# Kernel tuning notes

Hardware: AMD Instinct MI355X
Metric: run time of the kernel (lower is better)

Reference implementation:

```python
import jax, jax.numpy as jnp
import numpy as np

B, T, S, G, D, H, W, CHUNK = 2, 4096, 4096, 64, 1024, 16, 512, 256
HD = D // H


def setup_inputs() -> dict:
    key = jax.random.key(0)
    ks = jax.random.split(key, 16)
    std = 1.0 / np.sqrt(D)
    w = lambda k: jax.random.normal(k, (D, D), jnp.float32) * std
    b = lambda k: jax.random.normal(k, (D,), jnp.float32) * 0.01
    return {
        "query": jax.random.normal(ks[0], (B, T, D), jnp.float32),
        "encoder_out": jax.random.normal(ks[1], (B, S, D), jnp.float32),
        "global_tokens": jax.random.normal(ks[2], (B, G, D), jnp.float32),
        "qw": w(ks[3]), "qb": b(ks[4]),
        "kw": w(ks[5]), "kb": b(ks[6]),
        "vw": w(ks[7]), "vb": b(ks[8]),
        "gkw": w(ks[9]), "gkb": b(ks[10]),
        "gvw": w(ks[11]), "gvb": b(ks[12]),
        "ow": w(ks[13]), "ob": b(ks[14]),
        "compression_ratio": 1,
    }


def reference(query, encoder_out, global_tokens, qw, qb, kw, kb, vw, vb,
              gkw, gkb, gvw, gvb, ow, ob, compression_ratio):
    scale = jnp.float32(np.sqrt(HD))
    r = jnp.float32(compression_ratio)
    # expected raw position for each decoder step, clamped to valid src range
    expected = jnp.clip((jnp.arange(T, dtype=jnp.float32) / r).astype(jnp.int32), 0, S - 1)
    expected = jnp.broadcast_to(expected[None], (B, T))  # [B,T]

    lin = lambda x, wt, bs: x @ wt.T + bs  # torch nn.Linear: y = x W^T + b
    q = lin(query, qw, qb).reshape(B, T, H, HD).transpose(0, 2, 1, 3)            # [B,H,T,HD]
    gk = lin(global_tokens, gkw, gkb).reshape(B, G, H, HD).transpose(0, 2, 1, 3)  # [B,H,G,HD]
    gv = lin(global_tokens, gvw, gvb).reshape(B, G, H, HD).transpose(0, 2, 1, 3)
    ak = lin(encoder_out, kw, kb).reshape(B, S, H, HD).transpose(0, 2, 1, 3)      # [B,H,S,HD]
    av = lin(encoder_out, vw, vb).reshape(B, S, H, HD).transpose(0, 2, 1, 3)

    nC = T // CHUNK
    # per-(batch,chunk) window start, from the middle query's expected position
    centers = expected.reshape(B, nC, CHUNK)[:, :, CHUNK // 2]   # [B,nC]
    win_start = jnp.clip(centers - W // 2, 0, S - W)             # [B,nC]; window always full length W
    idx = win_start[:, :, None] + jnp.arange(W)[None, None, :]   # [B,nC,W]

    gather = lambda kv_b, idx_b: kv_b[:, idx_b, :]               # [H,S,HD],[nC,W] -> [H,nC,W,HD]
    wk = jax.vmap(gather)(ak, idx)                               # [B,H,nC,W,HD]
    wv = jax.vmap(gather)(av, idx)

    qc = q.reshape(B, H, nC, CHUNK, HD)
    sg = jnp.einsum('bhcqd,bhgd->bhcqg', qc, gk) / scale          # global scores  [B,H,nC,CHUNK,G]
    sl = jnp.einsum('bhcqd,bhcwd->bhcqw', qc, wk) / scale         # windowed scores [B,H,nC,CHUNK,W]
    attn = jax.nn.softmax(jnp.concatenate([sg, sl], axis=-1), axis=-1)
    out = (jnp.einsum('bhcqg,bhgd->bhcqd', attn[..., :G], gv)
           + jnp.einsum('bhcqw,bhcwd->bhcqd', attn[..., G:], wv))  # [B,H,nC,CHUNK,HD]
    out = out.reshape(B, H, T, HD).transpose(0, 2, 1, 3).reshape(B, T, D)
    return lin(out, ow, ob)
```

## Files before the change

### kernel.cpp

```cpp
#include <hip/hip_runtime.h>

typedef unsigned short u16;
typedef unsigned int u32;
typedef __attribute__((ext_vector_type(4))) float f32x4;
typedef __attribute__((ext_vector_type(16))) float f32x16;
typedef __attribute__((ext_vector_type(8))) short bf16x8;

constexpr int B_ = 2, T_ = 4096, S_ = 4096, G_ = 64, D_ = 1024, H_ = 16, W_ = 512, CHUNK_ = 256;
constexpr int NC_ = T_ / CHUNK_;
constexpr int NT_ = (G_ + W_) / 32;

__device__ __forceinline__ u16 f2bf(float x) {
  u32 u = __builtin_bit_cast(u32, x);
  return (u16)((u + 0x7FFFu + ((u >> 16) & 1u)) >> 16);
}

__global__ __launch_bounds__(256) void cvt_all_kernel(const float* __restrict__ q, const float* __restrict__ e,
                                                      const float* __restrict__ g, const float* __restrict__ w0,
                                                      const float* __restrict__ w1, const float* __restrict__ w2,
                                                      const float* __restrict__ w3, const float* __restrict__ w4,
                                                      const float* __restrict__ w5, u16* __restrict__ dst) {
  int blk = blockIdx.x;
  const float* src;
  int sblk;
  if (blk < 8192) { src = q; sblk = 0; }
  else if (blk < 16384) { src = e; sblk = 8192; }
  else if (blk < 16512) { src = g; sblk = 16384; }
  else if (blk < 17536) { src = w0; sblk = 16512; }
  else if (blk < 18560) { src = w1; sblk = 17536; }
  else if (blk < 19584) { src = w2; sblk = 18560; }
  else if (blk < 20608) { src = w3; sblk = 19584; }
  else if (blk < 21632) { src = w4; sblk = 20608; }
  else { src = w5; sblk = 21632; }
  int li = (blk - sblk) * 256 + threadIdx.x;
  size_t gi = (size_t)blk * 256 + threadIdx.x;
  float4 v = ((const float4*)src)[li];
  uint2 o;
  o.x = (u32)f2bf(v.x) | ((u32)f2bf(v.y) << 16);
  o.y = (u32)f2bf(v.z) | ((u32)f2bf(v.w) << 16);
  ((uint2*)dst)[gi] = o;
}

template <int MODE>
__global__ __launch_bounds__(256) void gemm_kernel(const u16* __restrict__ A, const u16* __restrict__ Bt,
                                                   const float* __restrict__ bias, const float* __restrict__ bias2,
                                                   size_t split, void* __restrict__ out) {
  __shared__ char lds[32768];
  char* As = lds;
  char* Bs = lds + 16384;
  const int tid = threadIdx.x;
  const int lane = tid & 63;
  const int wv = tid >> 6;
  const int wr = wv >> 1, wc = wv & 1;
  const int l15 = lane & 15, kg = lane >> 4;
  const int row0 = blockIdx.x * 128;
  const int col0 = blockIdx.y * 128;

  f32x4 acc[4][4];
#pragma unroll
  for (int i = 0; i < 4; i++)
#pragma unroll
    for (int j = 0; j < 4; j++)
#pragma unroll
      for (int r = 0; r < 4; r++) acc[i][j][r] = 0.f;

  const char* Abase = (const char*)A;
  const char* Bbase = (const char*)Bt;

  const int kb = 16 * ((lane & 3) ^ ((lane >> 3) & 3));
  auto stage = [&](int bufsel, int k0) {
#pragma unroll
    for (int c = 0; c < 2; c++) {
      int arow = wv * 32 + c * 16 + (lane >> 2);
      int dsto = bufsel * 8192 + wv * 2048 + c * 1024 + lane * 16;
      const char* ga = Abase + ((size_t)(row0 + arow) * 2048 + (size_t)k0 * 2 + kb);
      __builtin_amdgcn_global_load_lds((const __attribute__((address_space(1))) void*)ga,
                                       (__attribute__((address_space(3))) void*)(As + dsto), 16, 0, 0);
      const char* gb = Bbase + ((size_t)(col0 + arow) * 2048 + (size_t)k0 * 2 + kb);
      __builtin_amdgcn_global_load_lds((const __attribute__((address_space(1))) void*)gb,
                                       (__attribute__((address_space(3))) void*)(Bs + dsto), 16, 0, 0);
    }
  };

  stage(0, 0);
  __syncthreads();

  for (int it = 0; it < 32; ++it) {
    const int cur = it & 1;
    if (it + 1 < 32) stage(cur ^ 1, (it + 1) * 32);

    const char* Ab = As + cur * 8192;
    const char* Bb = Bs + cur * 8192;
    bf16x8 af[4], bfv[4];
#pragma unroll
    for (int mi = 0; mi < 4; mi++) {
      int row = wr * 64 + mi * 16 + l15;
      af[mi] = *(const bf16x8*)(Ab + ((row * 64 + kg * 16) ^ ((row & 6) << 3)));
    }
#pragma unroll
    for (int ni = 0; ni < 4; ni++) {
      int row = wc * 64 + ni * 16 + l15;
      bfv[ni] = *(const bf16x8*)(Bb + ((row * 64 + kg * 16) ^ ((row & 6) << 3)));
    }
    __builtin_amdgcn_s_setprio(1);
#pragma unroll
    for (int mi = 0; mi < 4; mi++)
#pragma unroll
      for (int ni = 0; ni < 4; ni++)
        acc[mi][ni] = __builtin_amdgcn_mfma_f32_16x16x32_bf16(bfv[ni], af[mi], acc[mi][ni], 0, 0, 0);
    __builtin_amdgcn_s_setprio(0);
    __syncthreads();
  }

  const float* bp = bias;
  size_t obase = 0;
  if (MODE == 3 && col0 >= 1024) {
    bp = bias2 - 1024;
    obase = split - 1024;
  }
  float4 bv4[4];
#pragma unroll
  for (int ni = 0; ni < 4; ni++) bv4[ni] = *(const float4*)&bp[col0 + wc * 64 + ni * 16 + kg * 4];
#pragma unroll
  for (int mi = 0; mi < 4; mi++) {
    size_t grow = (size_t)(row0 + wr * 64 + mi * 16 + l15);
#pragma unroll
    for (int ni = 0; ni < 4; ni++) {
      int gcol = col0 + wc * 64 + ni * 16 + kg * 4;
      float v0 = acc[mi][ni][0] + bv4[ni].x;
      float v1 = acc[mi][ni][1] + bv4[ni].y;
      float v2 = acc[mi][ni][2] + bv4[ni].z;
      float v3 = acc[mi][ni][3] + bv4[ni].w;
      if (MODE == 1) {
        v0 *= 0.18033688011112042f; v1 *= 0.18033688011112042f;
        v2 *= 0.18033688011112042f; v3 *= 0.18033688011112042f;
      }
      if (MODE == 2) {
        float4 fo = {v0, v1, v2, v3};
        *(float4*)&((float*)out)[grow * 1024 + gcol] = fo;
      } else {
        uint2 o;
        asm("v_cvt_pk_bf16_f32 %0, %1, %2" : "=v"(o.x) : "v"(v0), "v"(v1));
        asm("v_cvt_pk_bf16_f32 %0, %1, %2" : "=v"(o.y) : "v"(v2), "v"(v3));
        *(uint2*)&((u16*)out)[obase + grow * 1024 + gcol] = o;
      }
    }
  }
}

template <int MODE>
__global__ __launch_bounds__(512, 2) void gemm256_kernel(const u16* __restrict__ A, const u16* __restrict__ Bt,
                                                         const float* __restrict__ bias, const float* __restrict__ bias2,
                                                         size_t split, void* __restrict__ out) {
  __shared__ char lds[98304];
  const int tid = threadIdx.x;
  const int lane = tid & 63;
  const int wid = tid >> 6;
  const int wm = wid >> 2, wn = wid & 3;
  const int l15 = lane & 15, kg = lane >> 4;
  const int bid = blockIdx.x;
  const int swz = (bid & 7) * 32 + (bid >> 3);
  const int row0 = (swz & 31) * 256;
  const int col0 = (swz >> 5) * 256;

  f32x4 acc[8][4];
#pragma unroll
  for (int i = 0; i < 8; i++)
#pragma unroll
    for (int j = 0; j < 4; j++)
#pragma unroll
      for (int r = 0; r < 4; r++) acc[i][j][r] = 0.f;

  const char* Abase = (const char*)A;
  const char* Bbase = (const char*)Bt;
  const int kb = 16 * ((tid & 3) ^ ((tid >> 3) & 3));
  const int rl0 = tid >> 2;

  auto stageOp = [&](const char* base, int rowbase, int ldsbase, int kt) {
#pragma unroll
    for (int j = 0; j < 2; j++) {
      int dst = ldsbase + tid * 16 + j * 8192;
      const char* g = base + (size_t)(rowbase + rl0 + j * 128) * 2048 + kt * 64 + kb;
      __builtin_amdgcn_global_load_lds((const __attribute__((address_space(1))) void*)g,
                                       (__attribute__((address_space(3))) void*)(lds + dst), 16, 0, 0);
    }
  };

  stageOp(Abase, row0, 0, 0);
  stageOp(Bbase, col0, 49152, 0);
  stageOp(Abase, row0, 16384, 1);
  stageOp(Bbase, col0, 49152 + 16384, 1);
  asm volatile("s_waitcnt vmcnt(4)" ::: "memory");
  __builtin_amdgcn_s_barrier();

  int cur = 0, nx = 2;
  for (int t = 0; t < 32; ++t) {
    const char* Ab = lds + cur * 16384;
    const char* Bb = lds + 49152 + cur * 16384;
    bf16x8 bfv[4], af[4];
#pragma unroll
    for (int ni = 0; ni < 4; ni++) {
      int r = wn * 64 + ni * 16 + l15;
      bfv[ni] = *(const bf16x8*)(Bb + ((r * 64 + kg * 16) ^ (((r >> 1) & 3) << 4)));
    }
#pragma unroll
    for (int mi = 0; mi < 4; mi++) {
      int r = wm * 128 + mi * 16 + l15;
      af[mi] = *(const bf16x8*)(Ab + ((r * 64 + kg * 16) ^ (((r >> 1) & 3) << 4)));
    }
    if (t + 2 < 32) stageOp(Abase, row0, nx * 16384, t + 2);
    __builtin_amdgcn_s_barrier();
    __builtin_amdgcn_s_setprio(1);
#pragma unroll
    for (int mi = 0; mi < 4; mi++)
#pragma unroll
      for (int ni = 0; ni < 4; ni++)
        acc[mi][ni] = __builtin_amdgcn_mfma_f32_16x16x32_bf16(bfv[ni], af[mi], acc[mi][ni], 0, 0, 0);
    __builtin_amdgcn_s_setprio(0);
    __builtin_amdgcn_s_barrier();
#pragma unroll
    for (int mi = 0; mi < 4; mi++) {
      int r = wm * 128 + (mi + 4) * 16 + l15;
      af[mi] = *(const bf16x8*)(Ab + ((r * 64 + kg * 16) ^ (((r >> 1) & 3) << 4)));
    }
    if (t + 2 < 32) stageOp(Bbase, col0, 49152 + nx * 16384, t + 2);
    __builtin_amdgcn_s_barrier();
    __builtin_amdgcn_s_setprio(1);
#pragma unroll
    for (int mi = 0; mi < 4; mi++)
#pragma unroll
      for (int ni = 0; ni < 4; ni++)
        acc[mi + 4][ni] = __builtin_amdgcn_mfma_f32_16x16x32_bf16(bfv[ni], af[mi], acc[mi + 4][ni], 0, 0, 0);
    __builtin_amdgcn_s_setprio(0);
    if (t < 30) {
      asm volatile("s_waitcnt vmcnt(4)" ::: "memory");
    } else if (t == 30) {
      asm volatile("s_waitcnt vmcnt(0)" ::: "memory");
    }
    __builtin_amdgcn_s_barrier();
    cur = cur == 2 ? 0 : cur + 1;
    nx = nx == 2 ? 0 : nx + 1;
  }

  const float* bp = bias;
  size_t obase = 0;
  if (MODE == 3 && col0 >= 1024) {
    bp = bias2 - 1024;
    obase = split - 1024;
  }
  float4 bv4[4];
#pragma unroll
  for (int ni = 0; ni < 4; ni++) bv4[ni] = *(const float4*)&bp[col0 + wn * 64 + ni * 16 + kg * 4];
#pragma unroll
  for (int mi = 0; mi < 8; mi++) {
    size_t grow = (size_t)(row0 + wm * 128 + mi * 16 + l15);
#pragma unroll
    for (int ni = 0; ni < 4; ni++) {
      int gcol = col0 + wn * 64 + ni * 16 + kg * 4;
      float v0 = acc[mi][ni][0] + bv4[ni].x;
      float v1 = acc[mi][ni][1] + bv4[ni].y;
      float v2 = acc[mi][ni][2] + bv4[ni].z;
      float v3 = acc[mi][ni][3] + bv4[ni].w;
      if (MODE == 1) {
        v0 *= 0.18033688011112042f; v1 *= 0.18033688011112042f;
        v2 *= 0.18033688011112042f; v3 *= 0.18033688011112042f;
      }
      if (MODE == 2) {
        float4 fo = {v0, v1, v2, v3};
        *(float4*)&((float*)out)[grow * 1024 + gcol] = fo;
      } else {
        uint2 o;
        asm("v_cvt_pk_bf16_f32 %0, %1, %2" : "=v"(o.x) : "v"(v0), "v"(v1));
        asm("v_cvt_pk_bf16_f32 %0, %1, %2" : "=v"(o.y) : "v"(v2), "v"(v3));
        *(uint2*)&((u16*)out)[obase + grow * 1024 + gcol] = o;
      }
    }
  }
}

__global__ __launch_bounds__(512, 4) void attn_kernel(const u16* __restrict__ q_bf, const u16* __restrict__ k_bf,
                                                      const u16* __restrict__ v_bf, const u16* __restrict__ gk_bf,
                                                      const u16* __restrict__ gv_bf, u16* __restrict__ ao,
                                                      const int* __restrict__ rptr) {
  __shared__ u16 smem[16384];
  const int c = blockIdx.x, h = blockIdx.y, b = blockIdx.z;
  const int tid = threadIdx.x;
  const int lane = tid & 63, wv = tid >> 6;
  const int l31 = lane & 31, half = lane >> 5;
  const int t0 = c * CHUNK_;

  int rr = rptr[0];
  int centert = c * CHUNK_ + CHUNK_ / 2;
  int expected = (int)((float)centert / (float)rr);
  expected = min(max(expected, 0), S_ - 1);
  int ws0 = min(max(expected - W_ / 2, 0), S_ - W_);

  bf16x8 qf[4];
  {
    const u16* qrow = q_bf + ((size_t)(b * T_ + t0 + wv * 32 + l31)) * D_ + h * 64 + half * 8;
#pragma unroll
    for (int s = 0; s < 4; s++) qf[s] = *(const bf16x8*)(qrow + s * 16);
  }

  const int skey = (tid & 255) >> 3, shq = tid & 7;
  const bool isK = tid < 256;

  auto load_tile = [&](int j) -> uint4 {
    const u16* base;
    size_t row;
    if (j < 2) {
      base = isK ? gk_bf : gv_bf;
      row = (size_t)(b * G_ + j * 32 + skey);
    } else {
      base = isK ? k_bf : v_bf;
      row = (size_t)(b * S_ + ws0 + (j - 2) * 32 + skey);
    }
    return *(const uint4*)(base + row * D_ + h * 64 + shq * 8);
  };

  f32x16 oacc[2];
#pragma unroll
  for (int i = 0; i < 2; i++)
#pragma unroll
    for (int r = 0; r < 16; r++) oacc[i][r] = 0.f;
  float mrun = -1e30f, lsum = 0.f;

  uint4 stg = load_tile(0);

  for (int j = 0; j < NT_; j++) {
    const int bsel = j & 1;
    if (isK) {
      *(uint4*)((char*)smem + bsel * 4096 + ((skey * 128 + shq * 16) ^ ((skey & 7) << 4))) = stg;
    } else {
      const u16* pv = (const u16*)&stg;
      char* bp = (char*)smem + 8192 + bsel * 5248 + shq * 656 + skey * 2;
#pragma unroll
      for (int e = 0; e < 8; e++) *(u16*)(bp + e * 80) = pv[e];
    }
    if (j + 1 < NT_) stg = load_tile(j + 1);
    __syncthreads();

    const int kbase = bsel * 4096;
    const int vtb = 8192 + bsel * 5248;

    f32x16 sacc;
#pragma unroll
    for (int r = 0; r < 16; r++) sacc[r] = 0.f;
    __builtin_amdgcn_s_setprio(1);
#pragma unroll
    for (int s = 0; s < 4; s++) {
      int kbx = kbase + ((l31 * 128 + half * 16 + s * 32) ^ ((l31 & 7) << 4));
      bf16x8 kf = *(const bf16x8*)((char*)smem + kbx);
      sacc = __builtin_amdgcn_mfma_f32_32x32x16_bf16(kf, qf[s], sacc, 0, 0, 0);
    }
    __builtin_amdgcn_s_setprio(0);

    float t0m = fmaxf(fmaxf(sacc[0], sacc[1]), sacc[2]);
    float t1m = fmaxf(fmaxf(sacc[3], sacc[4]), sacc[5]);
    float t2m = fmaxf(fmaxf(sacc[6], sacc[7]), sacc[8]);
    float t3m = fmaxf(fmaxf(sacc[9], sacc[10]), sacc[11]);
    float t4m = fmaxf(fmaxf(sacc[12], sacc[13]), sacc[14]);
    float tmax = fmaxf(fmaxf(fmaxf(t0m, t1m), fmaxf(t2m, t3m)), fmaxf(t4m, sacc[15]));
    tmax = fmaxf(tmax, __shfl_xor(tmax, 32));
    if (__any(tmax > mrun + 8.f)) {
      float mnew = fmaxf(mrun, tmax);
      float fac = __builtin_amdgcn_exp2f(mrun - mnew);
      mrun = mnew;
      lsum *= fac;
#pragma unroll
      for (int i = 0; i < 2; i++)
#pragma unroll
        for (int r = 0; r < 16; r++) oacc[i][r] *= fac;
    }
    float p[16];
#pragma unroll
    for (int r = 0; r < 16; r++) p[r] = __builtin_amdgcn_exp2f(sacc[r] - mrun);
    float s0s = (p[0] + p[1]) + (p[2] + p[3]);
    float s1s = (p[4] + p[5]) + (p[6] + p[7]);
    float s2s = (p[8] + p[9]) + (p[10] + p[11]);
    float s3s = (p[12] + p[13]) + (p[14] + p[15]);
    float tsum = (s0s + s1s) + (s2s + s3s);
    tsum += __shfl_xor(tsum, 32);
    lsum += tsum;

    u32 xs[8], px[8];
#pragma unroll
    for (int i = 0; i < 8; i++)
      asm("v_cvt_pk_bf16_f32 %0, %1, %2" : "=v"(xs[i]) : "v"(p[2 * i]), "v"(p[2 * i + 1]));
#pragma unroll
    for (int i = 0; i < 8; i++) px[i] = (u32)__shfl_xor((int)xs[i], 32);
    u32 Bk[2][4];
    Bk[0][0] = half ? px[2] : xs[0];
    Bk[0][1] = half ? px[3] : xs[1];
    Bk[0][2] = half ? xs[2] : px[0];
    Bk[0][3] = half ? xs[3] : px[1];
    Bk[1][0] = half ? px[6] : xs[4];
    Bk[1][1] = half ? px[7] : xs[5];
    Bk[1][2] = half ? xs[6] : px[4];
    Bk[1][3] = half ? xs[7] : px[5];

    int vro = vtb + l31 * 80 + ((l31 >> 3) << 4) + half * 16;
    __builtin_amdgcn_s_setprio(1);
#pragma unroll
    for (int hdf = 0; hdf < 2; hdf++) {
#pragma unroll
      for (int ks = 0; ks < 2; ks++) {
        bf16x8 vf = *(const bf16x8*)((const char*)smem + vro + hdf * 2624 + ks * 32);
        uint4 u4;
        u4.x = Bk[ks][0]; u4.y = Bk[ks][1]; u4.z = Bk[ks][2]; u4.w = Bk[ks][3];
        bf16x8 pb = __builtin_bit_cast(bf16x8, u4);
        oacc[hdf] = __builtin_amdgcn_mfma_f32_32x32x16_bf16(vf, pb, oacc[hdf], 0, 0, 0);
      }
    }
    __builtin_amdgcn_s_setprio(0);
  }

  __syncthreads();
  float inv = 1.f / lsum;
#pragma unroll
  for (int hdf = 0; hdf < 2; hdf++) {
#pragma unroll
    for (int a = 0; a < 4; a++) {
      float f0 = oacc[hdf][4 * a] * inv, f1 = oacc[hdf][4 * a + 1] * inv;
      float f2 = oacc[hdf][4 * a + 2] * inv, f3 = oacc[hdf][4 * a + 3] * inv;
      uint2 o;
      asm("v_cvt_pk_bf16_f32 %0, %1, %2" : "=v"(o.x) : "v"(f0), "v"(f1));
      asm("v_cvt_pk_bf16_f32 %0, %1, %2" : "=v"(o.y) : "v"(f2), "v"(f3));
      int off = wv * 4096 + l31 * 128 + ((16 * a + 8 * half + 64 * hdf) ^ ((l31 & 7) << 4));
      *(uint2*)((char*)smem + off) = o;
    }
  }
  __syncthreads();
#pragma unroll
  for (int it = 0; it < 4; it++) {
    int byteo = (tid + it * 512) * 16;
    int row = byteo >> 7;
    int colb = byteo & 127;
    uint4 vv = *(const uint4*)((const char*)smem + row * 128 + (colb ^ ((row & 7) << 4)));
    *(uint4*)(ao + ((size_t)(b * T_ + t0 + row)) * D_ + h * 64 + (colb >> 1)) = vv;
  }
}

extern "C" void kernel_launch(void* const* d_in, const int* in_sizes, int n_in,
                              void* d_out, int out_size, void* d_ws, size_t ws_size,
                              hipStream_t stream) {
  (void)in_sizes; (void)n_in; (void)out_size; (void)ws_size;
  const float* query = (const float*)d_in[0];
  const float* enc = (const float*)d_in[1];
  const float* glob = (const float*)d_in[2];
  const float* qw = (const float*)d_in[3];
  const float* qb = (const float*)d_in[4];
  const float* kw = (const float*)d_in[5];
  const float* kb = (const float*)d_in[6];
  const float* vw = (const float*)d_in[7];
  const float* vb = (const float*)d_in[8];
  const float* gkw = (const float*)d_in[9];
  const float* gkb = (const float*)d_in[10];
  const float* gvw = (const float*)d_in[11];
  const float* gvb = (const float*)d_in[12];
  const float* ow = (const float*)d_in[13];
  const float* ob = (const float*)d_in[14];
  const int* rp = (const int*)d_in[15];

  const size_t NQ = (size_t)B_ * T_ * D_;
  const size_t NG = (size_t)B_ * G_ * D_;
  const size_t NW = (size_t)D_ * D_;

  u16* ws = (u16*)d_ws;
  u16* qx = ws;
  u16* ex = qx + NQ;
  u16* gx = ex + NQ;
  u16* wgt = gx + NG;
  u16* q_bf = wgt + 6 * NW;
  u16* k_bf = q_bf + NQ;
  u16* v_bf = k_bf + NQ;
  u16* gk_bf = v_bf + NQ;
  u16* gv_bf = gk_bf + NG;
  u16* ao = gv_bf + NG;

  cvt_all_kernel<<<22656, 256, 0, stream>>>(query, enc, glob, qw, kw, vw, gkw, gvw, ow, ws);

  gemm_kernel<1><<<dim3(64, 8), 256, 0, stream>>>(qx, wgt + 0 * NW, qb, qb, 0, q_bf);
  gemm256_kernel<3><<<256, 512, 0, stream>>>(ex, wgt + 1 * NW, kb, vb, NQ, k_bf);
  gemm_kernel<3><<<dim3(1, 16), 256, 0, stream>>>(gx, wgt + 3 * NW, gkb, gvb, NG, gk_bf);

  attn_kernel<<<dim3(NC_, H_, B_), 512, 0, stream>>>(q_bf, k_bf, v_bf, gk_bf, gv_bf, ao, rp);

  gemm_kernel<2><<<dim3(64, 8), 256, 0, stream>>>(ao, wgt + 5 * NW, ob, ob, 0, d_out);
}
```

Before: 164.2 us.

## Merge Q, K/V and global-token projections into one grouped GEMM launch

The separate Q projection GEMM, the 256x256-tile K/V GEMM and the small global-token GEMM are replaced by a single proj_kernel launch of 784 blocks. Each block picks its operand set, bias and output from its block index and computes a 256x128 tile with a triple-buffered direct-to-LDS pipeline. The aim is to remove launch gaps and fill the tail of one GEMM with work from the others. In exchange, K/V now uses smaller 128-column tiles with less B reuse. The global-token tile stages 256 rows of A while only 128 exist, so it reads past the gx buffer into adjacent workspace and discards those rows.

```diff
diff --git a/kernel.cpp b/kernel.cpp
--- a/kernel.cpp
+++ b/kernel.cpp
@@ -41,6 +41,163 @@
   ((uint2*)dst)[gi] = o;
 }
 
+__global__ __launch_bounds__(256, 2) void proj_kernel(const u16* __restrict__ ex, const u16* __restrict__ qx,
+                                                      const u16* __restrict__ gx, const u16* __restrict__ wgt,
+                                                      const float* __restrict__ qb, const float* __restrict__ kbias,
+                                                      const float* __restrict__ vbias, const float* __restrict__ gkb,
+                                                      const float* __restrict__ gvb, u16* __restrict__ q_bf,
+                                                      u16* __restrict__ k_bf, u16* __restrict__ gk_bf) {
+  __shared__ char lds[73728];
+  constexpr size_t NW = (size_t)D_ * D_;
+  constexpr size_t NQs = (size_t)B_ * T_ * D_;
+  constexpr size_t NGs = (size_t)B_ * G_ * D_;
+  const int tid = threadIdx.x;
+  const int lane = tid & 63;
+  const int wid = tid >> 6;
+  const int wm = wid >> 1, wn = wid & 1;
+  const int l15 = lane & 15, kg = lane >> 4;
+
+  const int bid = blockIdx.x;
+  const u16 *A, *Bt;
+  const float *b1, *b2;
+  u16* out;
+  int row0, col0, mloc;
+  bool scale = false, dual = false;
+  size_t dsplit = 0;
+  if (bid < 512) {
+    row0 = (bid & 31) * 256; col0 = (bid >> 5) * 128; mloc = 256;
+    A = ex; Bt = wgt + NW; b1 = kbias; b2 = vbias; out = k_bf; dsplit = NQs; dual = true;
+  } else if (bid < 768) {
+    int i = bid - 512;
+    row0 = (i & 31) * 256; col0 = (i >> 5) * 128; mloc = 256;
+    A = qx; Bt = wgt; b1 = qb; b2 = qb; out = q_bf; scale = true;
+  } else {
+    int i = bid - 768;
+    row0 = 0; col0 = i * 128; mloc = 128;
+    A = gx; Bt = wgt + 3 * NW; b1 = gkb; b2 = gvb; out = gk_bf; dsplit = NGs; dual = true;
+  }
+  const float* bp = b1;
+  u16* op = out;
+  if (dual && col0 >= 1024) { bp = b2 - 1024; op = out + (dsplit - 1024); }
+
+  f32x4 acc[8][4];
+#pragma unroll
+  for (int i = 0; i < 8; i++)
+#pragma unroll
+    for (int j = 0; j < 4; j++)
+#pragma unroll
+      for (int r = 0; r < 4; r++) acc[i][j][r] = 0.f;
+
+  const char* Abase = (const char*)A;
+  const char* Bbase = (const char*)Bt;
+  const int swb = 16 * ((tid & 3) ^ ((tid >> 3) & 3));
+
+  auto stageA = [&](int slot, int kt) {
+#pragma unroll
+    for (int p = 0; p < 4; p++) {
+      int dst = slot * 16384 + p * 4096 + tid * 16;
+      const char* g = Abase + (size_t)(row0 + p * 64 + (tid >> 2)) * 2048 + kt * 64 + swb;
+      __builtin_amdgcn_global_load_lds((const __attribute__((address_space(1))) void*)g,
+                                       (__attribute__((address_space(3))) void*)(lds + dst), 16, 0, 0);
+    }
+  };
+  auto stageB = [&](int slot, int kt) {
+#pragma unroll
+    for (int p = 0; p < 2; p++) {
+      int dst = 49152 + slot * 8192 + p * 4096 + tid * 16;
+      const char* g = Bbase + (size_t)(col0 + p * 64 + (tid >> 2)) * 2048 + kt * 64 + swb;
+      __builtin_amdgcn_global_load_lds((const __attribute__((address_space(1))) void*)g,
+                                       (__attribute__((address_space(3))) void*)(lds + dst), 16, 0, 0);
+    }
+  };
+
+  stageA(0, 0); stageB(0, 0);
+  stageA(1, 1); stageB(1, 1);
+  asm volatile("s_waitcnt vmcnt(6)" ::: "memory");
+  __builtin_amdgcn_s_barrier();
+
+  int cur = 0, nx = 2;
+  for (int t = 0; t < 32; ++t) {
+    const char* Ab = lds + cur * 16384;
+    const char* Bb = lds + 49152 + cur * 8192;
+    bf16x8 bfv[2], af[4];
+#pragma unroll
+    for (int ni = 0; ni < 2; ni++) {
+      int r = wn * 64 + ni * 16 + l15;
+      (void)r;
+    }
+    bf16x8 bq[4];
+#pragma unroll
+    for (int ni = 0; ni < 4; ni++) {
+      int r = wn * 64 + ni * 16 + l15;
+      bq[ni] = *(const bf16x8*)(Bb + ((r * 64 + kg * 16) ^ (((r >> 1) & 3) << 4)));
+    }
+#pragma unroll
+    for (int mi = 0; mi < 4; mi++) {
+      int r = wm * 128 + mi * 16 + l15;
+      af[mi] = *(const bf16x8*)(Ab + ((r * 64 + kg * 16) ^ (((r >> 1) & 3) << 4)));
+    }
+    if (t + 2 < 32) stageA(nx, t + 2);
+    __builtin_amdgcn_s_barrier();
+    __builtin_amdgcn_s_setprio(1);
+#pragma unroll
+    for (int mi = 0; mi < 4; mi++)
+#pragma unroll
+      for (int ni = 0; ni < 4; ni++)
+        acc[mi][ni] = __builtin_amdgcn_mfma_f32_16x16x32_bf16(bq[ni], af[mi], acc[mi][ni], 0, 0, 0);
+    __builtin_amdgcn_s_setprio(0);
+    __builtin_amdgcn_s_barrier();
+#pragma unroll
+    for (int mi = 0; mi < 4; mi++) {
+      int r = wm * 128 + (mi + 4) * 16 + l15;
+      af[mi] = *(const bf16x8*)(Ab + ((r * 64 + kg * 16) ^ (((r >> 1) & 3) << 4)));
+    }
+    if (t + 2 < 32) stageB(nx, t + 2);
+    __builtin_amdgcn_s_barrier();
+    __builtin_amdgcn_s_setprio(1);
+#pragma unroll
+    for (int mi = 0; mi < 4; mi++)
+#pragma unroll
+      for (int ni = 0; ni < 4; ni++)
+        acc[mi + 4][ni] = __builtin_amdgcn_mfma_f32_16x16x32_bf16(bq[ni], af[mi], acc[mi + 4][ni], 0, 0, 0);
+    __builtin_amdgcn_s_setprio(0);
+    if (t < 30) {
+      asm volatile("s_waitcnt vmcnt(6)" ::: "memory");
+    } else if (t == 30) {
+      asm volatile("s_waitcnt vmcnt(0)" ::: "memory");
+    }
+    __builtin_amdgcn_s_barrier();
+    cur = cur == 2 ? 0 : cur + 1;
+    nx = nx == 2 ? 0 : nx + 1;
+  }
+
+  float4 bv4[4];
+#pragma unroll
+  for (int ni = 0; ni < 4; ni++) bv4[ni] = *(const float4*)&bp[col0 + wn * 64 + ni * 16 + kg * 4];
+#pragma unroll
+  for (int mi = 0; mi < 8; mi++) {
+    int rloc = wm * 128 + mi * 16 + l15;
+    if (rloc >= mloc) continue;
+    size_t grow = (size_t)(row0 + rloc);
+#pragma unroll
+    for (int ni = 0; ni < 4; ni++) {
+      int gcol = col0 + wn * 64 + ni * 16 + kg * 4;
+      float v0 = acc[mi][ni][0] + bv4[ni].x;
+      float v1 = acc[mi][ni][1] + bv4[ni].y;
+      float v2 = acc[mi][ni][2] + bv4[ni].z;
+      float v3 = acc[mi][ni][3] + bv4[ni].w;
+      if (scale) {
+        v0 *= 0.18033688011112042f; v1 *= 0.18033688011112042f;
+        v2 *= 0.18033688011112042f; v3 *= 0.18033688011112042f;
+      }
+      uint2 o;
+      asm("v_cvt_pk_bf16_f32 %0, %1, %2" : "=v"(o.x) : "v"(v0), "v"(v1));
+      asm("v_cvt_pk_bf16_f32 %0, %1, %2" : "=v"(o.y) : "v"(v2), "v"(v3));
+      *(uint2*)&op[grow * 1024 + gcol] = o;
+    }
+  }
+}
+
 template <int MODE>
 __global__ __launch_bounds__(256) void gemm_kernel(const u16* __restrict__ A, const u16* __restrict__ Bt,
                                                    const float* __restrict__ bias, const float* __restrict__ bias2,
@@ -113,11 +270,7 @@
   }
 
   const float* bp = bias;
-  size_t obase = 0;
-  if (MODE == 3 && col0 >= 1024) {
-    bp = bias2 - 1024;
-    obase = split - 1024;
-  }
+  (void)bias2; (void)split;
   float4 bv4[4];
 #pragma unroll
   for (int ni = 0; ni < 4; ni++) bv4[ni] = *(const float4*)&bp[col0 + wc * 64 + ni * 16 + kg * 4];
@@ -131,10 +284,6 @@
       float v1 = acc[mi][ni][1] + bv4[ni].y;
       float v2 = acc[mi][ni][2] + bv4[ni].z;
       float v3 = acc[mi][ni][3] + bv4[ni].w;
-      if (MODE == 1) {
-        v0 *= 0.18033688011112042f; v1 *= 0.18033688011112042f;
-        v2 *= 0.18033688011112042f; v3 *= 0.18033688011112042f;
-      }
       if (MODE == 2) {
         float4 fo = {v0, v1, v2, v3};
         *(float4*)&((float*)out)[grow * 1024 + gcol] = fo;
@@ -142,137 +291,7 @@
         uint2 o;
         asm("v_cvt_pk_bf16_f32 %0, %1, %2" : "=v"(o.x) : "v"(v0), "v"(v1));
         asm("v_cvt_pk_bf16_f32 %0, %1, %2" : "=v"(o.y) : "v"(v2), "v"(v3));
-        *(uint2*)&((u16*)out)[obase + grow * 1024 + gcol] = o;
-      }
-    }
-  }
-}
-
-template <int MODE>
-__global__ __launch_bounds__(512, 2) void gemm256_kernel(const u16* __restrict__ A, const u16* __restrict__ Bt,
-                                                         const float* __restrict__ bias, const float* __restrict__ bias2,
-                                                         size_t split, void* __restrict__ out) {
-  __shared__ char lds[98304];
-  const int tid = threadIdx.x;
-  const int lane = tid & 63;
-  const int wid = tid >> 6;
-  const int wm = wid >> 2, wn = wid & 3;
-  const int l15 = lane & 15, kg = lane >> 4;
-  const int bid = blockIdx.x;
-  const int swz = (bid & 7) * 32 + (bid >> 3);
-  const int row0 = (swz & 31) * 256;
-  const int col0 = (swz >> 5) * 256;
-
-  f32x4 acc[8][4];
-#pragma unroll
-  for (int i = 0; i < 8; i++)
-#pragma unroll
-    for (int j = 0; j < 4; j++)
-#pragma unroll
-      for (int r = 0; r < 4; r++) acc[i][j][r] = 0.f;
-
-  const char* Abase = (const char*)A;
-  const char* Bbase = (const char*)Bt;
-  const int kb = 16 * ((tid & 3) ^ ((tid >> 3) & 3));
-  const int rl0 = tid >> 2;
-
-  auto stageOp = [&](const char* base, int rowbase, int ldsbase, int kt) {
-#pragma unroll
-    for (int j = 0; j < 2; j++) {
-      int dst = ldsbase + tid * 16 + j * 8192;
-      const char* g = base + (size_t)(rowbase + rl0 + j * 128) * 2048 + kt * 64 + kb;
-      __builtin_amdgcn_global_load_lds((const __attribute__((address_space(1))) void*)g,
-                                       (__attribute__((address_space(3))) void*)(lds + dst), 16, 0, 0);
-    }
-  };
-
-  stageOp(Abase, row0, 0, 0);
-  stageOp(Bbase, col0, 49152, 0);
-  stageOp(Abase, row0, 16384, 1);
-  stageOp(Bbase, col0, 49152 + 16384, 1);
-  asm volatile("s_waitcnt vmcnt(4)" ::: "memory");
-  __builtin_amdgcn_s_barrier();
-
-  int cur = 0, nx = 2;
-  for (int t = 0; t < 32; ++t) {
-    const char* Ab = lds + cur * 16384;
-    const char* Bb = lds + 49152 + cur * 16384;
-    bf16x8 bfv[4], af[4];
-#pragma unroll
-    for (int ni = 0; ni < 4; ni++) {
-      int r = wn * 64 + ni * 16 + l15;
-      bfv[ni] = *(const bf16x8*)(Bb + ((r * 64 + kg * 16) ^ (((r >> 1) & 3) << 4)));
-    }
-#pragma unroll
-    for (int mi = 0; mi < 4; mi++) {
-      int r = wm * 128 + mi * 16 + l15;
-      af[mi] = *(const bf16x8*)(Ab + ((r * 64 + kg * 16) ^ (((r >> 1) & 3) << 4)));
-    }
-    if (t + 2 < 32) stageOp(Abase, row0, nx * 16384, t + 2);
-    __builtin_amdgcn_s_barrier();
-    __builtin_amdgcn_s_setprio(1);
-#pragma unroll
-    for (int mi = 0; mi < 4; mi++)
-#pragma unroll
-      for (int ni = 0; ni < 4; ni++)
-        acc[mi][ni] = __builtin_amdgcn_mfma_f32_16x16x32_bf16(bfv[ni], af[mi], acc[mi][ni], 0, 0, 0);
-    __builtin_amdgcn_s_setprio(0);
-    __builtin_amdgcn_s_barrier();
-#pragma unroll
-    for (int mi = 0; mi < 4; mi++) {
-      int r = wm * 128 + (mi + 4) * 16 + l15;
-      af[mi] = *(const bf16x8*)(Ab + ((r * 64 + kg * 16) ^ (((r >> 1) & 3) << 4)));
-    }
-    if (t + 2 < 32) stageOp(Bbase, col0, 49152 + nx * 16384, t + 2);
-    __builtin_amdgcn_s_barrier();
-    __builtin_amdgcn_s_setprio(1);
-#pragma unroll
-    for (int mi = 0; mi < 4; mi++)
-#pragma unroll
-      for (int ni = 0; ni < 4; ni++)
-        acc[mi + 4][ni] = __builtin_amdgcn_mfma_f32_16x16x32_bf16(bfv[ni], af[mi], acc[mi + 4][ni], 0, 0, 0);
-    __builtin_amdgcn_s_setprio(0);
-    if (t < 30) {
-      asm volatile("s_waitcnt vmcnt(4)" ::: "memory");
-    } else if (t == 30) {
-      asm volatile("s_waitcnt vmcnt(0)" ::: "memory");
-    }
-    __builtin_amdgcn_s_barrier();
-    cur = cur == 2 ? 0 : cur + 1;
-    nx = nx == 2 ? 0 : nx + 1;
-  }
-
-  const float* bp = bias;
-  size_t obase = 0;
-  if (MODE == 3 && col0 >= 1024) {
-    bp = bias2 - 1024;
-    obase = split - 1024;
-  }
-  float4 bv4[4];
-#pragma unroll
-  for (int ni = 0; ni < 4; ni++) bv4[ni] = *(const float4*)&bp[col0 + wn * 64 + ni * 16 + kg * 4];
-#pragma unroll
-  for (int mi = 0; mi < 8; mi++) {
-    size_t grow = (size_t)(row0 + wm * 128 + mi * 16 + l15);
-#pragma unroll
-    for (int ni = 0; ni < 4; ni++) {
-      int gcol = col0 + wn * 64 + ni * 16 + kg * 4;
-      float v0 = acc[mi][ni][0] + bv4[ni].x;
-      float v1 = acc[mi][ni][1] + bv4[ni].y;
-      float v2 = acc[mi][ni][2] + bv4[ni].z;
-      float v3 = acc[mi][ni][3] + bv4[ni].w;
-      if (MODE == 1) {
-        v0 *= 0.18033688011112042f; v1 *= 0.18033688011112042f;
-        v2 *= 0.18033688011112042f; v3 *= 0.18033688011112042f;
-      }
-      if (MODE == 2) {
-        float4 fo = {v0, v1, v2, v3};
-        *(float4*)&((float*)out)[grow * 1024 + gcol] = fo;
-      } else {
-        uint2 o;
-        asm("v_cvt_pk_bf16_f32 %0, %1, %2" : "=v"(o.x) : "v"(v0), "v"(v1));
-        asm("v_cvt_pk_bf16_f32 %0, %1, %2" : "=v"(o.y) : "v"(v2), "v"(v3));
-        *(uint2*)&((u16*)out)[obase + grow * 1024 + gcol] = o;
+        *(uint2*)&((u16*)out)[grow * 1024 + gcol] = o;
       }
     }
   }
@@ -480,9 +499,7 @@
 
   cvt_all_kernel<<<22656, 256, 0, stream>>>(query, enc, glob, qw, kw, vw, gkw, gvw, ow, ws);
 
-  gemm_kernel<1><<<dim3(64, 8), 256, 0, stream>>>(qx, wgt + 0 * NW, qb, qb, 0, q_bf);
-  gemm256_kernel<3><<<256, 512, 0, stream>>>(ex, wgt + 1 * NW, kb, vb, NQ, k_bf);
-  gemm_kernel<3><<<dim3(1, 16), 256, 0, stream>>>(gx, wgt + 3 * NW, gkb, gvb, NG, gk_bf);
+  proj_kernel<<<784, 256, 0, stream>>>(ex, qx, gx, wgt, qb, kb, vb, gkb, gvb, q_bf, k_bf, gk_bf);
 
   attn_kernel<<<dim3(NC_, H_, B_), 512, 0, stream>>>(q_bf, k_bf, v_bf, gk_bf, gv_bf, ao, rp);
 
```

Result: faster. 151.6 us (-7.7%).
